# Kernel optimization log

Measured on AMD Instinct MI355X. Metric: run time of the kernel, lower is better.

## Reference

```python
import jax, jax.numpy as jnp
import numpy as np

D_MODEL = 1024
H = 16
D_HEAD = D_MODEL // H  # 64


def setup_inputs() -> dict:
    key = jax.random.key(0)
    ks = jax.random.split(key, 11)
    B, L = 4, 1024
    s = 0.02
    return {
        "Q": jax.random.normal(ks[0], (B, L, D_MODEL), jnp.float32),
        "K": jax.random.normal(ks[1], (B, L, D_MODEL), jnp.float32),
        "V": jax.random.normal(ks[2], (B, L, D_MODEL), jnp.float32),
        # per-head Dense weights stacked on a leading head axis (Keras Dense: y = x @ W + b)
        "Wq": jax.random.normal(ks[3], (H, D_MODEL, D_HEAD), jnp.float32) * s,
        "bq": jnp.zeros((H, D_HEAD), jnp.float32),
        "Wk": jax.random.normal(ks[4], (H, D_MODEL, D_HEAD), jnp.float32) * s,
        "bk": jnp.zeros((H, D_HEAD), jnp.float32),
        "Wv": jax.random.normal(ks[5], (H, D_MODEL, D_HEAD), jnp.float32) * s,
        "bv": jnp.zeros((H, D_HEAD), jnp.float32),
        "Wo": jax.random.normal(ks[6], (D_MODEL, D_MODEL), jnp.float32) * s,
        "bo": jnp.zeros((D_MODEL,), jnp.float32),
    }


def reference(Q, K, V, Wq, bq, Wk, bk, Wv, bv, Wo, bo):
    # per-head projections, vectorized over heads: [B, H, L, Dh]
    q = jnp.einsum("bld,hde->bhle", Q, Wq) + bq[None, :, None, :]
    k = jnp.einsum("bld,hde->bhle", K, Wk) + bk[None, :, None, :]
    v = jnp.einsum("bld,hde->bhle", V, Wv) + bv[None, :, None, :]
    # scaled dot-product attention scores: [B, H, Lq, Lk]
    scores = jnp.einsum("bhqe,bhke->bhqk", q, k) / jnp.sqrt(jnp.asarray(D_HEAD, q.dtype))
    attn = jax.nn.softmax(scores, axis=-1)
    out_h = jnp.einsum("bhqk,bhke->bhqe", attn, v)  # [B, H, Lq, Dh]
    # concat heads along feature dim (matches tf.concat(heads, axis=2))
    B, Hh, Lq, Dh = out_h.shape
    concat = out_h.transpose(0, 2, 1, 3).reshape(B, Lq, Hh * Dh)
    output = concat @ Wo + bo
    # tf.stack(heads_attention) -> [H, B, Lq, Lk]
    attention = attn.transpose(1, 0, 2, 3)
    return output, attention
```

## Files before the change

### kernel.cpp

```cpp
#include <hip/hip_runtime.h>
#include <stdint.h>

#define DEVI __device__ __forceinline__
typedef unsigned short u16;
typedef __attribute__((ext_vector_type(8))) short s16x8;
typedef __attribute__((ext_vector_type(4))) float f32x4;

typedef __attribute__((address_space(1))) void as1_void;
typedef __attribute__((address_space(3))) void as3_void;

DEVI u16 f2b(float f){
  union { float f; uint32_t u; } x; x.f = f;
  return (u16)((x.u + 0x7fffu + ((x.u >> 16) & 1u)) >> 16);
}

DEVI void gload16(const void* g, void* l){
  __builtin_amdgcn_global_load_lds((as1_void*)g, (as3_void*)l, 16, 0, 0);
}

DEVI f32x4 MFMA(s16x8 a, s16x8 b, f32x4 c){
  return __builtin_amdgcn_mfma_f32_16x16x32_bf16(a, b, c, 0, 0, 0);
}

__global__ __launch_bounds__(256)
void k_prep(const float* __restrict__ Q, const float* __restrict__ Kc,
            const float* __restrict__ V,
            u16* __restrict__ Qb, u16* __restrict__ Kb, u16* __restrict__ Vb,
            const float* __restrict__ Wq, const float* __restrict__ Wk,
            const float* __restrict__ Wv, const float* __restrict__ Wo,
            u16* __restrict__ WqT, u16* __restrict__ WkT,
            u16* __restrict__ WvT, u16* __restrict__ WoT){
  __shared__ float t[64][65];
  const int bid = blockIdx.x, tid = threadIdx.x;
  if(bid < 12288){
    int tno = bid >> 12;
    int blk = bid & 4095;
    const float* s = (tno == 0) ? Q : (tno == 1) ? Kc : V;
    u16* d = (tno == 0) ? Qb : (tno == 1) ? Kb : Vb;
    int i = (blk * 256 + tid) * 4;
    float4 v = *(const float4*)(s + i);
    ushort4 o;
    o.x = f2b(v.x); o.y = f2b(v.y); o.z = f2b(v.z); o.w = f2b(v.w);
    *(ushort4*)(d + i) = o;
  } else {
    int j = bid - 12288;
    const float* src; u16* dst; int C, r0, c0;
    const int R = 1024;
    if(j < 768){
      int tno = j >> 8, rem = j & 255;
      int head = rem >> 4, rt = rem & 15;
      src = ((tno == 0) ? Wq : (tno == 1) ? Wk : Wv) + head * 65536;
      dst = ((tno == 0) ? WqT : (tno == 1) ? WkT : WvT) + head * 65536;
      C = 64; r0 = rt * 64; c0 = 0;
    } else {
      int j2 = j - 768;
      src = Wo; dst = WoT; C = 1024;
      r0 = (j2 & 15) * 64; c0 = (j2 >> 4) * 64;
    }
    int tx = tid & 63, ty = tid >> 6;
    #pragma unroll
    for(int i = 0; i < 64; i += 4)
      t[ty + i][tx] = src[(size_t)(r0 + ty + i) * C + c0 + tx];
    __syncthreads();
    #pragma unroll
    for(int i = 0; i < 64; i += 4)
      dst[(size_t)(c0 + ty + i) * R + r0 + tx] = f2b(t[tx][ty + i]);
  }
}

template<int BM>
DEVI void gemm_core(int mode, const u16* __restrict__ A, const u16* __restrict__ Bt,
                    const float* __restrict__ bias, void* __restrict__ Cp,
                    int m0, int n0, u16* sAb, u16* sBb){
  const int tid = threadIdx.x, w = tid >> 6, l = tid & 63;
  const int wr = w >> 1, wc = w & 1;
  constexpr int MI = BM / 32;
  f32x4 acc[MI][4];
  #pragma unroll
  for(int a = 0; a < MI; a++)
    #pragma unroll
    for(int b = 0; b < 4; b++) acc[a][b] = (f32x4){0.f, 0.f, 0.f, 0.f};

  const int NT = 16;
  auto STAGE = [&](int buf, int t){
    #pragma unroll
    for(int s2 = 0; s2 < BM / 32; s2++){
      int s = (BM / 32) * w + s2;
      int r = s * 8 + (l >> 3);
      int ch = (l & 7) ^ (r & 7);
      gload16((const char*)A + ((size_t)(m0 + r) * 1024 + t * 64) * 2 + ch * 16,
              (char*)(sAb + (size_t)buf * BM * 64) + s * 1024 + l * 16);
    }
    #pragma unroll
    for(int s2 = 0; s2 < 4; s2++){
      int s = 4 * w + s2;
      int r = s * 8 + (l >> 3);
      int ch = (l & 7) ^ (r & 7);
      gload16((const char*)Bt + ((size_t)(n0 + r) * 1024 + t * 64) * 2 + ch * 16,
              (char*)(sBb + (size_t)buf * 8192) + s * 1024 + l * 16);
    }
  };
  STAGE(0, 0);
  __syncthreads();
  for(int t = 0; t < NT; t++){
    const int cur = t & 1;
    if(t + 1 < NT) STAGE(cur ^ 1, t + 1);
    const char* pa = (const char*)(sAb + (size_t)cur * BM * 64);
    const char* pb = (const char*)(sBb + (size_t)cur * 8192);
    s16x8 af[MI][2], bf[4][2];
    #pragma unroll
    for(int mi = 0; mi < MI; mi++){
      int r = (BM / 2) * wr + 16 * mi + (l & 15);
      #pragma unroll
      for(int kk = 0; kk < 2; kk++)
        af[mi][kk] = *(const s16x8*)(pa + r * 128 + ((kk * 64 + 16 * (l >> 4)) ^ ((r & 7) << 4)));
    }
    #pragma unroll
    for(int ni = 0; ni < 4; ni++){
      int r = 64 * wc + 16 * ni + (l & 15);
      #pragma unroll
      for(int kk = 0; kk < 2; kk++)
        bf[ni][kk] = *(const s16x8*)(pb + r * 128 + ((kk * 64 + 16 * (l >> 4)) ^ ((r & 7) << 4)));
    }
    #pragma unroll
    for(int kk = 0; kk < 2; kk++)
      #pragma unroll
      for(int mi = 0; mi < MI; mi++)
        #pragma unroll
        for(int ni = 0; ni < 4; ni++)
          acc[mi][ni] = MFMA(af[mi][kk], bf[ni][kk], acc[mi][ni]);
    __syncthreads();
  }
  #pragma unroll
  for(int mi = 0; mi < MI; mi++){
    #pragma unroll
    for(int ni = 0; ni < 4; ni++){
      #pragma unroll
      for(int i = 0; i < 4; i++){
        int gr = m0 + (BM / 2) * wr + 16 * mi + 4 * (l >> 4) + i;
        int gc = n0 + 64 * wc + 16 * ni + (l & 15);
        float v = acc[mi][ni][i];
        if(mode == 0){
          ((u16*)Cp)[(size_t)gr * 1024 + gc] = f2b(v + bias[gc]);
        } else if(mode == 1){
          ((u16*)Cp)[((size_t)(gc >> 10) << 20) + ((size_t)gr << 10) + (gc & 1023)] =
              f2b(v + bias[gr]);
        } else {
          ((float*)Cp)[(size_t)gr * 1024 + gc] = v + bias[gc];
        }
      }
    }
  }
}

__global__ __launch_bounds__(256)
void k_proj(const u16* __restrict__ Qb, const u16* __restrict__ Kb,
            const u16* __restrict__ Vb,
            const u16* __restrict__ WqT, const u16* __restrict__ WkT,
            const u16* __restrict__ WvT,
            const float* __restrict__ bq, const float* __restrict__ bk,
            const float* __restrict__ bv,
            u16* __restrict__ q_ws, u16* __restrict__ k_ws, u16* __restrict__ vT_ws){
  __shared__ u16 sA[2][128 * 64];
  __shared__ u16 sB[2][128 * 64];
  const int bid = blockIdx.x;
  if(bid < 256){
    gemm_core<128>(0, Qb, WqT, bq, q_ws, (bid >> 3) * 128, (bid & 7) * 128,
                   &sA[0][0], &sB[0][0]);
  } else if(bid < 512){
    int b2 = bid - 256;
    gemm_core<128>(0, Kb, WkT, bk, k_ws, (b2 >> 3) * 128, (b2 & 7) * 128,
                   &sA[0][0], &sB[0][0]);
  } else {
    int b2 = bid - 512;
    gemm_core<128>(1, WvT, Vb, bv, vT_ws, (b2 >> 5) * 128, (b2 & 31) * 128,
                   &sA[0][0], &sB[0][0]);
  }
}

__global__ __launch_bounds__(256)
void k_final(const u16* __restrict__ A, const u16* __restrict__ Bt,
             const float* __restrict__ bias, float* __restrict__ C){
  __shared__ u16 sA[2][64 * 64];
  __shared__ u16 sB[2][128 * 64];
  const int bid = blockIdx.x;
  gemm_core<64>(2, A, Bt, bias, C, (bid >> 3) * 64, (bid & 7) * 128,
                &sA[0][0], &sB[0][0]);
}

__global__ __launch_bounds__(256)
void k_attn(const u16* __restrict__ qws, const u16* __restrict__ kws,
            const u16* __restrict__ vws, float* __restrict__ attn,
            u16* __restrict__ concat){
  __shared__ u16 q_s[64 * 64];
  __shared__ u16 k_s[128 * 64];
  __shared__ u16 v_s[64 * 128];
  __shared__ u16 p_s[64 * 128];
  const int tid = threadIdx.x, w = tid >> 6, l = tid & 63;
  const int bx = blockIdx.x;
  const int bh = bx & 63, qb = bx >> 6, b = bh >> 4, h = bh & 15;
  const char* qg = (const char*)qws + ((size_t)(b * 1024 + qb * 64) * 1024 + h * 64) * 2;
  const char* kg = (const char*)kws + ((size_t)(b * 1024) * 1024 + h * 64) * 2;
  const char* vg = (const char*)vws + ((size_t)b * 1048576 + (size_t)h * 64 * 1024) * 2;
  float* ao = attn + (size_t)((h * 4 + b) * 1024 + qb * 64) * 1024;
  u16* cw = concat + (size_t)(b * 1024 + qb * 64) * 1024 + h * 64;

  #pragma unroll
  for(int s2 = 0; s2 < 2; s2++){
    int s = 2 * w + s2;
    int r = s * 8 + (l >> 3);
    int ch = (l & 7) ^ (r & 7);
    gload16(qg + (size_t)r * 2048 + ch * 16, (char*)q_s + s * 1024 + l * 16);
  }

  const float KS = 0.18033688011112042f;
  float rs[4] = {0.f, 0.f, 0.f, 0.f};
  s16x8 af0, af1;

  for(int kt = 0; kt < 8; kt++){
    __syncthreads();
    #pragma unroll
    for(int s2 = 0; s2 < 4; s2++){
      int s = 4 * w + s2;
      int r = s * 8 + (l >> 3);
      int ch = (l & 7) ^ (r & 7);
      gload16(kg + (size_t)(kt * 128 + r) * 2048 + ch * 16, (char*)k_s + s * 1024 + l * 16);
    }
    __syncthreads();
    if(kt == 0){
      int rq = 16 * w + (l & 15);
      af0 = *(const s16x8*)((const char*)q_s + rq * 128 + ((16 * (l >> 4)) ^ ((rq & 7) << 4)));
      af1 = *(const s16x8*)((const char*)q_s + rq * 128 + ((64 + 16 * (l >> 4)) ^ ((rq & 7) << 4)));
    }
    #pragma unroll
    for(int f = 0; f < 8; f++){
      int r = 16 * f + (l & 15);
      s16x8 b0 = *(const s16x8*)((const char*)k_s + r * 128 + ((16 * (l >> 4)) ^ ((r & 7) << 4)));
      s16x8 b1 = *(const s16x8*)((const char*)k_s + r * 128 + ((64 + 16 * (l >> 4)) ^ ((r & 7) << 4)));
      f32x4 sf = (f32x4){0.f, 0.f, 0.f, 0.f};
      sf = MFMA(af0, b0, sf);
      sf = MFMA(af1, b1, sf);
      #pragma unroll
      for(int i = 0; i < 4; i++) rs[i] += exp2f(sf[i] * KS);
    }
  }
  #pragma unroll
  for(int i = 0; i < 4; i++){
    #pragma unroll
    for(int m = 1; m < 16; m <<= 1) rs[i] += __shfl_xor(rs[i], m, 64);
  }
  float inv[4];
  #pragma unroll
  for(int i = 0; i < 4; i++) inv[i] = 1.0f / rs[i];

  f32x4 oacc[4];
  #pragma unroll
  for(int fe = 0; fe < 4; fe++) oacc[fe] = (f32x4){0.f, 0.f, 0.f, 0.f};

  for(int kt = 0; kt < 8; kt++){
    __syncthreads();
    #pragma unroll
    for(int s2 = 0; s2 < 4; s2++){
      int s = 4 * w + s2;
      int r = s * 8 + (l >> 3);
      int ch = (l & 7) ^ (r & 7);
      gload16(kg + (size_t)(kt * 128 + r) * 2048 + ch * 16, (char*)k_s + s * 1024 + l * 16);
    }
    #pragma unroll
    for(int s2 = 0; s2 < 4; s2++){
      int s = 4 * w + s2;
      int e = s * 4 + (l >> 4);
      int ch = (l & 15) ^ (e & 15);
      gload16(vg + (size_t)e * 2048 + (size_t)kt * 256 + ch * 16, (char*)v_s + s * 1024 + l * 16);
    }
    __syncthreads();
    f32x4 sf[8];
    #pragma unroll
    for(int f = 0; f < 8; f++){
      int r = 16 * f + (l & 15);
      s16x8 b0 = *(const s16x8*)((const char*)k_s + r * 128 + ((16 * (l >> 4)) ^ ((r & 7) << 4)));
      s16x8 b1 = *(const s16x8*)((const char*)k_s + r * 128 + ((64 + 16 * (l >> 4)) ^ ((r & 7) << 4)));
      sf[f] = (f32x4){0.f, 0.f, 0.f, 0.f};
      sf[f] = MFMA(af0, b0, sf[f]);
      sf[f] = MFMA(af1, b1, sf[f]);
    }
    #pragma unroll
    for(int f = 0; f < 8; f++){
      #pragma unroll
      for(int i = 0; i < 4; i++){
        float p = exp2f(sf[f][i] * KS) * inv[i];
        int rr = 16 * w + 4 * (l >> 4) + i;
        ao[(size_t)rr * 1024 + kt * 128 + 16 * f + (l & 15)] = p;
        *(u16*)((char*)p_s + rr * 256 + (((16 * f + (l & 15)) * 2) ^ ((rr & 15) << 4))) = f2b(p);
      }
    }
    __syncthreads();
    #pragma unroll
    for(int kc = 0; kc < 4; kc++){
      int rp = 16 * w + (l & 15);
      s16x8 pa = *(const s16x8*)((const char*)p_s + rp * 256 + ((kc * 64 + 16 * (l >> 4)) ^ ((rp & 15) << 4)));
      #pragma unroll
      for(int fe = 0; fe < 4; fe++){
        int e = 16 * fe + (l & 15);
        s16x8 bv = *(const s16x8*)((const char*)v_s + e * 256 + ((kc * 64 + 16 * (l >> 4)) ^ ((e & 15) << 4)));
        oacc[fe] = MFMA(pa, bv, oacc[fe]);
      }
    }
  }
  #pragma unroll
  for(int fe = 0; fe < 4; fe++){
    #pragma unroll
    for(int i = 0; i < 4; i++){
      int qi = 16 * w + 4 * (l >> 4) + i;
      cw[(size_t)qi * 1024 + 16 * fe + (l & 15)] = f2b(oacc[fe][i]);
    }
  }
}

extern "C" void kernel_launch(void* const* d_in, const int* in_sizes, int n_in,
                              void* d_out, int out_size, void* d_ws, size_t ws_size,
                              hipStream_t stream){
  const float* Q  = (const float*)d_in[0];
  const float* Kc = (const float*)d_in[1];
  const float* V  = (const float*)d_in[2];
  const float* Wq = (const float*)d_in[3];
  const float* bq = (const float*)d_in[4];
  const float* Wk = (const float*)d_in[5];
  const float* bk = (const float*)d_in[6];
  const float* Wv = (const float*)d_in[7];
  const float* bv = (const float*)d_in[8];
  const float* Wo = (const float*)d_in[9];
  const float* bo = (const float*)d_in[10];
  float* out = (float*)d_out;

  char* ws = (char*)d_ws;
  u16* q_ws      = (u16*)(ws + 0);
  u16* k_ws      = (u16*)(ws + 8388608);
  u16* vT_ws     = (u16*)(ws + 16777216);
  u16* concat_ws = (u16*)(ws + 25165824);
  u16* WqT = (u16*)(ws + 33554432);
  u16* WkT = (u16*)(ws + 35651584);
  u16* WvT = (u16*)(ws + 37748736);
  u16* WoT = (u16*)(ws + 39845888);

  u16* Qb = (u16*)((char*)d_out + 16777216);
  u16* Kb = (u16*)((char*)d_out + 25165824);
  u16* Vb = (u16*)((char*)d_out + 33554432);
  float* attn = out + 4194304;

  k_prep<<<13312, 256, 0, stream>>>(Q, Kc, V, Qb, Kb, Vb,
                                    Wq, Wk, Wv, Wo, WqT, WkT, WvT, WoT);
  k_proj<<<768, 256, 0, stream>>>(Qb, Kb, Vb, WqT, WkT, WvT, bq, bk, bv,
                                  q_ws, k_ws, vT_ws);
  k_attn<<<1024, 256, 0, stream>>>(q_ws, k_ws, vT_ws, attn, concat_ws);
  k_final<<<512, 256, 0, stream>>>(concat_ws, WoT, bo, out);
}
```

Measured before the change: 191.5 us.

## Cache unnormalized scores in LDS to avoid recomputing QK^T, remap GEMM blocks

The attention kernel previously computed QK^T twice: once for row sums and again for the normalized probabilities. It now computes QK^T once, keeps the bf16 exponentials for the full 64x1024 tile in LDS, and runs P·V on the unnormalized values, scaling by 1/rowsum at the end. K and V are staged in 64-row double-buffered tiles, and the attention output is written from LDS with vectorized float4 stores. The projection and final GEMMs also remap block IDs to change L2 locality. In exchange, the attention probabilities are now rounded to bf16 before being written as fp32, which loses precision. The 128KB+ of LDS per block also limits occupancy to one block per CU.

```diff
diff --git a/kernel.cpp b/kernel.cpp
--- a/kernel.cpp
+++ b/kernel.cpp
@@ -12,6 +12,10 @@
 DEVI u16 f2b(float f){
   union { float f; uint32_t u; } x; x.f = f;
   return (u16)((x.u + 0x7fffu + ((x.u >> 16) & 1u)) >> 16);
+}
+DEVI float b2f(u16 u){
+  union { uint32_t u; float f; } x; x.u = ((uint32_t)u) << 16;
+  return x.f;
 }
 
 DEVI void gload16(const void* g, void* l){
@@ -163,7 +167,8 @@
             u16* __restrict__ q_ws, u16* __restrict__ k_ws, u16* __restrict__ vT_ws){
   __shared__ u16 sA[2][128 * 64];
   __shared__ u16 sB[2][128 * 64];
-  const int bid = blockIdx.x;
+  const int raw = blockIdx.x;
+  const int bid = (raw & 7) * 96 + (raw >> 3);
   if(bid < 256){
     gemm_core<128>(0, Qb, WqT, bq, q_ws, (bid >> 3) * 128, (bid & 7) * 128,
                    &sA[0][0], &sB[0][0]);
@@ -183,7 +188,8 @@
              const float* __restrict__ bias, float* __restrict__ C){
   __shared__ u16 sA[2][64 * 64];
   __shared__ u16 sB[2][128 * 64];
-  const int bid = blockIdx.x;
+  const int raw = blockIdx.x;
+  const int bid = (raw & 7) * 64 + (raw >> 3);
   gemm_core<64>(2, A, Bt, bias, C, (bid >> 3) * 64, (bid & 7) * 128,
                 &sA[0][0], &sB[0][0]);
 }
@@ -192,10 +198,10 @@
 void k_attn(const u16* __restrict__ qws, const u16* __restrict__ kws,
             const u16* __restrict__ vws, float* __restrict__ attn,
             u16* __restrict__ concat){
+  __shared__ u16 S_s[64 * 1024];
   __shared__ u16 q_s[64 * 64];
-  __shared__ u16 k_s[128 * 64];
-  __shared__ u16 v_s[64 * 128];
-  __shared__ u16 p_s[64 * 128];
+  __shared__ u16 kv_s[2][64 * 64];
+  __shared__ float inv_s[64];
   const int tid = threadIdx.x, w = tid >> 6, l = tid & 63;
   const int bx = blockIdx.x;
   const int bh = bx & 63, qb = bx >> 6, b = bh >> 4, h = bh & 15;
@@ -205,6 +211,25 @@
   float* ao = attn + (size_t)((h * 4 + b) * 1024 + qb * 64) * 1024;
   u16* cw = concat + (size_t)(b * 1024 + qb * 64) * 1024 + h * 64;
 
+  auto STAGEK = [&](int buf, int kt){
+    #pragma unroll
+    for(int rd = 0; rd < 2; rd++){
+      int c = rd * 256 + tid;
+      int r = c >> 3, ch8 = c & 7;
+      gload16(kg + (size_t)(kt * 64 + r) * 2048 + ((ch8 ^ (r & 7)) * 16),
+              (char*)&kv_s[buf][0] + c * 16);
+    }
+  };
+  auto STAGEV = [&](int buf, int kt){
+    #pragma unroll
+    for(int rd = 0; rd < 2; rd++){
+      int c = rd * 256 + tid;
+      int e = c >> 3, ch8 = c & 7;
+      gload16(vg + (size_t)e * 2048 + (size_t)kt * 128 + ((ch8 ^ (e & 7)) * 16),
+              (char*)&kv_s[buf][0] + c * 16);
+    }
+  };
+
   #pragma unroll
   for(int s2 = 0; s2 < 2; s2++){
     int s = 2 * w + s2;
@@ -212,107 +237,108 @@
     int ch = (l & 7) ^ (r & 7);
     gload16(qg + (size_t)r * 2048 + ch * 16, (char*)q_s + s * 1024 + l * 16);
   }
+  STAGEK(0, 0);
+  __syncthreads();
 
   const float KS = 0.18033688011112042f;
   float rs[4] = {0.f, 0.f, 0.f, 0.f};
   s16x8 af0, af1;
-
-  for(int kt = 0; kt < 8; kt++){
-    __syncthreads();
-    #pragma unroll
-    for(int s2 = 0; s2 < 4; s2++){
-      int s = 4 * w + s2;
-      int r = s * 8 + (l >> 3);
-      int ch = (l & 7) ^ (r & 7);
-      gload16(kg + (size_t)(kt * 128 + r) * 2048 + ch * 16, (char*)k_s + s * 1024 + l * 16);
-    }
-    __syncthreads();
-    if(kt == 0){
-      int rq = 16 * w + (l & 15);
-      af0 = *(const s16x8*)((const char*)q_s + rq * 128 + ((16 * (l >> 4)) ^ ((rq & 7) << 4)));
-      af1 = *(const s16x8*)((const char*)q_s + rq * 128 + ((64 + 16 * (l >> 4)) ^ ((rq & 7) << 4)));
-    }
-    #pragma unroll
-    for(int f = 0; f < 8; f++){
+  {
+    int rq = 16 * w + (l & 15);
+    af0 = *(const s16x8*)((const char*)q_s + rq * 128 + ((16 * (l >> 4)) ^ ((rq & 7) << 4)));
+    af1 = *(const s16x8*)((const char*)q_s + rq * 128 + ((64 + 16 * (l >> 4)) ^ ((rq & 7) << 4)));
+  }
+
+  for(int kt = 0; kt < 16; kt++){
+    const int cur = kt & 1;
+    if(kt + 1 < 16) STAGEK(cur ^ 1, kt + 1);
+    f32x4 sf[4];
+    #pragma unroll
+    for(int f = 0; f < 4; f++){
       int r = 16 * f + (l & 15);
-      s16x8 b0 = *(const s16x8*)((const char*)k_s + r * 128 + ((16 * (l >> 4)) ^ ((r & 7) << 4)));
-      s16x8 b1 = *(const s16x8*)((const char*)k_s + r * 128 + ((64 + 16 * (l >> 4)) ^ ((r & 7) << 4)));
-      f32x4 sf = (f32x4){0.f, 0.f, 0.f, 0.f};
-      sf = MFMA(af0, b0, sf);
-      sf = MFMA(af1, b1, sf);
-      #pragma unroll
-      for(int i = 0; i < 4; i++) rs[i] += exp2f(sf[i] * KS);
-    }
-  }
-  #pragma unroll
-  for(int i = 0; i < 4; i++){
-    #pragma unroll
-    for(int m = 1; m < 16; m <<= 1) rs[i] += __shfl_xor(rs[i], m, 64);
-  }
-  float inv[4];
-  #pragma unroll
-  for(int i = 0; i < 4; i++) inv[i] = 1.0f / rs[i];
-
-  f32x4 oacc[4];
-  #pragma unroll
-  for(int fe = 0; fe < 4; fe++) oacc[fe] = (f32x4){0.f, 0.f, 0.f, 0.f};
-
-  for(int kt = 0; kt < 8; kt++){
-    __syncthreads();
-    #pragma unroll
-    for(int s2 = 0; s2 < 4; s2++){
-      int s = 4 * w + s2;
-      int r = s * 8 + (l >> 3);
-      int ch = (l & 7) ^ (r & 7);
-      gload16(kg + (size_t)(kt * 128 + r) * 2048 + ch * 16, (char*)k_s + s * 1024 + l * 16);
-    }
-    #pragma unroll
-    for(int s2 = 0; s2 < 4; s2++){
-      int s = 4 * w + s2;
-      int e = s * 4 + (l >> 4);
-      int ch = (l & 15) ^ (e & 15);
-      gload16(vg + (size_t)e * 2048 + (size_t)kt * 256 + ch * 16, (char*)v_s + s * 1024 + l * 16);
-    }
-    __syncthreads();
-    f32x4 sf[8];
-    #pragma unroll
-    for(int f = 0; f < 8; f++){
-      int r = 16 * f + (l & 15);
-      s16x8 b0 = *(const s16x8*)((const char*)k_s + r * 128 + ((16 * (l >> 4)) ^ ((r & 7) << 4)));
-      s16x8 b1 = *(const s16x8*)((const char*)k_s + r * 128 + ((64 + 16 * (l >> 4)) ^ ((r & 7) << 4)));
+      s16x8 b0 = *(const s16x8*)((const char*)&kv_s[cur][0] + r * 128 + ((16 * (l >> 4)) ^ ((r & 7) << 4)));
+      s16x8 b1 = *(const s16x8*)((const char*)&kv_s[cur][0] + r * 128 + ((64 + 16 * (l >> 4)) ^ ((r & 7) << 4)));
       sf[f] = (f32x4){0.f, 0.f, 0.f, 0.f};
       sf[f] = MFMA(af0, b0, sf[f]);
       sf[f] = MFMA(af1, b1, sf[f]);
     }
     #pragma unroll
-    for(int f = 0; f < 8; f++){
+    for(int f = 0; f < 4; f++){
       #pragma unroll
       for(int i = 0; i < 4; i++){
-        float p = exp2f(sf[f][i] * KS) * inv[i];
+        float e = exp2f(sf[f][i] * KS);
+        rs[i] += e;
         int rr = 16 * w + 4 * (l >> 4) + i;
-        ao[(size_t)rr * 1024 + kt * 128 + 16 * f + (l & 15)] = p;
-        *(u16*)((char*)p_s + rr * 256 + (((16 * f + (l & 15)) * 2) ^ ((rr & 15) << 4))) = f2b(p);
+        int colb = kt * 128 + f * 32 + (l & 15) * 2;
+        *(u16*)((char*)S_s + rr * 2048 + (colb ^ ((rr & 15) << 4))) = f2b(e);
       }
     }
     __syncthreads();
-    #pragma unroll
-    for(int kc = 0; kc < 4; kc++){
-      int rp = 16 * w + (l & 15);
-      s16x8 pa = *(const s16x8*)((const char*)p_s + rp * 256 + ((kc * 64 + 16 * (l >> 4)) ^ ((rp & 15) << 4)));
+  }
+
+  #pragma unroll
+  for(int i = 0; i < 4; i++){
+    #pragma unroll
+    for(int m = 1; m < 16; m <<= 1) rs[i] += __shfl_xor(rs[i], m, 64);
+  }
+  float inv[4];
+  #pragma unroll
+  for(int i = 0; i < 4; i++) inv[i] = 1.0f / rs[i];
+  if((l & 15) == 0){
+    #pragma unroll
+    for(int i = 0; i < 4; i++) inv_s[16 * w + 4 * (l >> 4) + i] = inv[i];
+  }
+  STAGEV(0, 0);
+  __syncthreads();
+
+  f32x4 oacc[4];
+  #pragma unroll
+  for(int fe = 0; fe < 4; fe++) oacc[fe] = (f32x4){0.f, 0.f, 0.f, 0.f};
+  const int rp = 16 * w + (l & 15);
+  for(int kt = 0; kt < 16; kt++){
+    const int cur = kt & 1;
+    if(kt + 1 < 16) STAGEV(cur ^ 1, kt + 1);
+    #pragma unroll
+    for(int kc = 0; kc < 2; kc++){
+      s16x8 pa = *(const s16x8*)((const char*)S_s + rp * 2048 +
+                  ((kt * 128 + kc * 64 + 16 * (l >> 4)) ^ ((rp & 15) << 4)));
       #pragma unroll
       for(int fe = 0; fe < 4; fe++){
         int e = 16 * fe + (l & 15);
-        s16x8 bv = *(const s16x8*)((const char*)v_s + e * 256 + ((kc * 64 + 16 * (l >> 4)) ^ ((e & 15) << 4)));
+        s16x8 bv = *(const s16x8*)((const char*)&kv_s[cur][0] + e * 128 +
+                    ((kc * 64 + 16 * (l >> 4)) ^ ((e & 7) << 4)));
         oacc[fe] = MFMA(pa, bv, oacc[fe]);
       }
     }
-  }
+    __syncthreads();
+  }
+
   #pragma unroll
   for(int fe = 0; fe < 4; fe++){
     #pragma unroll
     for(int i = 0; i < 4; i++){
       int qi = 16 * w + 4 * (l >> 4) + i;
-      cw[(size_t)qi * 1024 + 16 * fe + (l & 15)] = f2b(oacc[fe][i]);
+      cw[(size_t)qi * 1024 + 16 * fe + (l & 15)] = f2b(oacc[fe][i] * inv[i]);
+    }
+  }
+
+  {
+    const int rrow = 16 * w + (l >> 2);
+    const float invr = inv_s[rrow];
+    const char* srow = (const char*)S_s + rrow * 2048;
+    float* arow = ao + (size_t)rrow * 1024;
+    const int cb0 = (l & 3) * 16;
+    #pragma unroll 4
+    for(int j = 0; j < 32; j++){
+      s16x8 pv = *(const s16x8*)(srow + ((j * 64 + cb0) ^ ((rrow & 15) << 4)));
+      float4 o0, o1;
+      o0.x = b2f((u16)pv[0]) * invr; o0.y = b2f((u16)pv[1]) * invr;
+      o0.z = b2f((u16)pv[2]) * invr; o0.w = b2f((u16)pv[3]) * invr;
+      o1.x = b2f((u16)pv[4]) * invr; o1.y = b2f((u16)pv[5]) * invr;
+      o1.z = b2f((u16)pv[6]) * invr; o1.w = b2f((u16)pv[7]) * invr;
+      float* p = arow + j * 32 + (l & 3) * 8;
+      *(float4*)p = o0;
+      *(float4*)(p + 4) = o1;
     }
   }
 }
```

Result: slower. 247.2 us (+29.1%).
